# Performance work log

Measured on AMD Instinct MI355X. Metric: run time of the kernel, lower is better.

The kernel has to match this reference:

```python
import jax, jax.numpy as jnp
import numpy as np

B, N, D, K = 8, 262144, 16, 256
M_MAX = 1024  # cap on condensation points per event for the pairwise repulsion block
ATTR_W, REP_W = 1.0, 1.0
BETA_POS_W, BETA_NEG_SIG_W, BETA_NEG_BG_W, MARGIN_W = 10.0, 3.0, 6.0, 10.0
THR, MARGIN = 0.5, 0.3
ALPHA, GAMMA = 0.75, 2.0


def setup_inputs() -> dict:
    key = jax.random.key(0)
    k1, k2, k3, k4 = jax.random.split(key, 4)
    beta = jax.random.normal(k1, (B, N, 1), jnp.float32)
    embed = jax.random.normal(k2, (B, N, D), jnp.float32)
    slice_id = jax.random.randint(k3, (B, N), -1, K)          # -1 == background
    is_cp = jax.random.uniform(k4, (B, N)) < 0.001            # sparse condensation points
    return {"beta": beta, "embed": embed, "slice_id": slice_id, "is_cp": is_cp}


def _per_event(beta, emb, sid, cp):
    # beta [N], emb [N,D], sid [N] int, cp [N] bool
    f32 = beta.dtype
    valid = sid >= 0
    cpv = cp & valid
    seg = jnp.where(valid, sid, K).astype(jnp.int32)          # slot K = invalid/background bucket

    p = jax.nn.sigmoid(beta)
    ce1 = jax.nn.softplus(-beta)   # BCE-with-logits, target = 1
    ce0 = jax.nn.softplus(beta)    # BCE-with-logits, target = 0

    # ---- pos_bce: size-weighted per-instance focal BCE over CP hits ----
    focal = ALPHA * (1.0 - p) ** GAMMA * ce1
    cpf = cp.astype(f32)
    sum_f = jax.ops.segment_sum(focal * cpf, seg, num_segments=K + 1)[:K]
    cnt_cp = jax.ops.segment_sum(cpf, seg, num_segments=K + 1)[:K]
    inst_size = jax.ops.segment_sum(jnp.ones_like(beta), seg, num_segments=K + 1)[:K]
    has_cp = cnt_cp > 0
    mean_f = sum_f / jnp.maximum(cnt_cp, 1.0)
    w = jnp.where(has_cp, inst_size, 0.0)
    pos_bce = jnp.sum(w * mean_f) / jnp.maximum(jnp.sum(w), 1.0)

    # ---- negative / background BCE and margin terms ----
    ncpf = (~cp).astype(f32)
    n_ncp = jnp.sum(ncpf)
    neg_bce = jnp.where(n_ncp > 0, jnp.sum(ce0 * ncpf) / jnp.maximum(n_ncp, 1.0), 0.0)
    n_cp = jnp.sum(cpf)
    pos_margin = jnp.sum(jax.nn.relu(THR + MARGIN - p) * cpf) / jnp.maximum(n_cp, 1.0)
    neg_margin = jnp.where(n_ncp > 0,
                           jnp.sum(jax.nn.relu(p - (THR - MARGIN)) * ncpf) / jnp.maximum(n_ncp, 1.0), 0.0)
    bgf = (sid == -1).astype(f32)
    n_bg = jnp.sum(bgf)
    bg_bce = jnp.where(n_bg > 0, jnp.sum(ce0 * bgf) / jnp.maximum(n_bg, 1.0), 0.0)

    beta_loss = (BETA_POS_W * pos_bce + BETA_NEG_SIG_W * neg_bce +
                 BETA_NEG_BG_W * bg_bce + MARGIN_W * (pos_margin + neg_margin))

    # ---- attraction: per-instance mean sq-dist to the FIRST CP hit of that instance ----
    idx = jnp.where(cp, jnp.arange(N), N)
    first_idx = jax.ops.segment_min(idx, seg, num_segments=K + 1)[:K]   # N if instance has no CP
    anchor_k = emb[jnp.clip(first_idx, 0, N - 1)]                       # [K,D]
    anchor = anchor_k[jnp.clip(sid, 0, K - 1)]                          # [N,D]
    d2 = jnp.sum((emb - anchor) ** 2, axis=-1)
    s_d2 = jax.ops.segment_sum(d2 * valid.astype(f32), seg, num_segments=K + 1)[:K]
    attraction = ATTR_W * jnp.sum(jnp.where(has_cp, s_d2 / jnp.maximum(inst_size, 1.0), 0.0))

    # ---- repulsion: mean exp(-||ci-cj||^2) over all CP x CP pairs (incl. diagonal) ----
    order = jnp.argsort(jnp.where(cpv, jnp.arange(N), N))[:M_MAX]
    selv = cpv[order].astype(f32)                                       # [M]
    cp_emb = emb[order]                                                 # [M,D]
    pd2 = jnp.sum((cp_emb[:, None, :] - cp_emb[None, :, :]) ** 2, axis=-1)
    Mv = jnp.sum(cpv.astype(f32))
    rep = jnp.sum(jnp.exp(-pd2) * (selv[:, None] * selv[None, :])) / jnp.maximum(Mv * Mv, 1.0)
    repulsion = jnp.where(Mv > 1, REP_W * rep, 0.0)

    loss = beta_loss + attraction + repulsion
    ok = (jnp.sum(valid) > 0) & (Mv > 0)
    return loss, ok


def reference(beta, embed, slice_id, is_cp):
    beta2 = beta[..., 0]  # squeeze(-1)
    loss_b, ok_b = jax.vmap(_per_event)(beta2, embed, slice_id, is_cp)
    cnt = jnp.sum(ok_b.astype(beta2.dtype))
    total = jnp.sum(jnp.where(ok_b, loss_b, 0.0))
    return jnp.where(cnt > 0, total / jnp.maximum(cnt, 1.0), 0.0)
```

## Files before the change

### kernel.cpp

```cpp
#include <hip/hip_runtime.h>
#include <math.h>

#define Bn 8
#define Nn 262144
#define Kk 256
#define Dd 16
#define MCAP 4096
#define MSEL 1024
#define CHUNK 4096
#define ASTRIDE 17

#define W_ATTR 1.0f
#define W_REP 1.0f
#define W_BPOS 10.0f
#define W_BNEG 3.0f
#define W_BBG 6.0f
#define W_MARG 10.0f
#define ALPHA_F 0.75f

#define OFF_SUMF   0
#define OFF_CNT    (Bn*Kk)
#define OFF_INST   (2*Bn*Kk)
#define OFF_FIRST  (3*Bn*Kk)
#define OFF_SD2    (4*Bn*Kk)
#define OFF_ANCH   (5*Bn*Kk)
#define OFF_SCAL   (OFF_ANCH + Bn*Kk*Dd)
#define OFF_CPIDX  (OFF_SCAL + Bn*16)
#define OFF_MODE   (OFF_CPIDX + Bn*MCAP)
#define WS_WORDS   (OFF_MODE + 1)

__global__ void k_init(int* wsi) {
  int stride = gridDim.x * blockDim.x;
  for (int i = blockIdx.x * blockDim.x + threadIdx.x; i < WS_WORDS; i += stride) {
    int v = 0;
    if (i >= OFF_FIRST && i < OFF_FIRST + Bn * Kk) v = 0x7FFFFFFF;
    wsi[i] = v;
  }
}

__global__ void k_detect(const unsigned int* w, int* wsi) {
  int stride = gridDim.x * blockDim.x;
  int bad = 0;
  for (int i = blockIdx.x * blockDim.x + threadIdx.x; i < (Bn * Nn) / 4; i += stride) {
    unsigned int x = w[i];
    if (x > 1u && x != 0x3F800000u) bad = 1;
  }
  if (bad) atomicOr(&wsi[OFF_MODE], 1);
}

__global__ __launch_bounds__(256) void k_pass1(const float* __restrict__ beta,
                                               const int* __restrict__ sid,
                                               const void* __restrict__ cpp,
                                               float* wsf, int* wsi) {
  const int b = blockIdx.y;
  const int tid = threadIdx.x;
  __shared__ float ls_sumf[Kk];
  __shared__ int ls_cnt[Kk], ls_inst[Kk], ls_first[Kk];
  __shared__ float sr[4][4];
  __shared__ float si[4][2];
  ls_sumf[tid] = 0.f; ls_cnt[tid] = 0; ls_inst[tid] = 0; ls_first[tid] = 0x7FFFFFFF;
  __syncthreads();
  const int mode = wsi[OFF_MODE];
  const int base = b * Nn;
  const int i0 = blockIdx.x * CHUNK;
  float a_ce0n = 0.f, a_rpos = 0.f, a_rneg = 0.f, a_ce0b = 0.f;
  float a_ncp = 0.f, a_nbg = 0.f;
  for (int it = 0; it < CHUNK / 256; ++it) {
    int i = i0 + it * 256 + tid;
    int s = sid[base + i];
    bool cp;
    if (mode) cp = ((const unsigned char*)cpp)[base + i] != 0;
    else      cp = ((const unsigned int*)cpp)[base + i] != 0u;
    float x = beta[base + i];
    float p = 1.f / (1.f + __expf(-x));
    float ax = fabsf(x);
    float sp = log1pf(__expf(-ax));
    float ce1 = sp + fmaxf(-x, 0.f);
    float ce0 = sp + fmaxf(x, 0.f);
    if (cp) { a_rpos += fmaxf(0.8f - p, 0.f); a_ncp += 1.f; }
    else { a_ce0n += ce0; a_rneg += fmaxf(p - 0.2f, 0.f); }
    if (s == -1) { a_ce0b += ce0; a_nbg += 1.f; }
    if (s >= 0) {
      atomicAdd(&ls_inst[s], 1);
      if (cp) {
        float om = 1.f - p;
        float focal = ALPHA_F * om * om * ce1;
        atomicAdd(&ls_sumf[s], focal);
        atomicAdd(&ls_cnt[s], 1);
        atomicMin(&ls_first[s], i);
        int pos = atomicAdd(&wsi[OFF_SCAL + b * 16 + 6], 1);
        if (pos < MCAP) wsi[OFF_CPIDX + b * MCAP + pos] = i;
      }
    }
  }
  __syncthreads();
  atomicAdd(&wsf[OFF_SUMF + b * Kk + tid], ls_sumf[tid]);
  atomicAdd(&wsi[OFF_CNT + b * Kk + tid], ls_cnt[tid]);
  atomicAdd(&wsi[OFF_INST + b * Kk + tid], ls_inst[tid]);
  atomicMin(&wsi[OFF_FIRST + b * Kk + tid], ls_first[tid]);
  for (int o = 32; o > 0; o >>= 1) {
    a_ce0n += __shfl_down(a_ce0n, o);
    a_rpos += __shfl_down(a_rpos, o);
    a_rneg += __shfl_down(a_rneg, o);
    a_ce0b += __shfl_down(a_ce0b, o);
    a_ncp  += __shfl_down(a_ncp, o);
    a_nbg  += __shfl_down(a_nbg, o);
  }
  int wv = tid >> 6;
  if ((tid & 63) == 0) {
    sr[wv][0] = a_ce0n; sr[wv][1] = a_rpos; sr[wv][2] = a_rneg; sr[wv][3] = a_ce0b;
    si[wv][0] = a_ncp;  si[wv][1] = a_nbg;
  }
  __syncthreads();
  if (tid == 0) {
    float s0 = 0, s1 = 0, s2 = 0, s3 = 0, s4 = 0, s5 = 0;
    for (int wq = 0; wq < 4; ++wq) {
      s0 += sr[wq][0]; s1 += sr[wq][1]; s2 += sr[wq][2]; s3 += sr[wq][3];
      s4 += si[wq][0]; s5 += si[wq][1];
    }
    atomicAdd(&wsf[OFF_SCAL + b * 16 + 0], s0);
    atomicAdd(&wsf[OFF_SCAL + b * 16 + 1], s1);
    atomicAdd(&wsf[OFF_SCAL + b * 16 + 2], s2);
    atomicAdd(&wsf[OFF_SCAL + b * 16 + 3], s3);
    atomicAdd(&wsf[OFF_SCAL + b * 16 + 4], s4);
    atomicAdd(&wsf[OFF_SCAL + b * 16 + 5], s5);
  }
}

__global__ __launch_bounds__(256) void k_event(const float* __restrict__ embed,
                                               float* wsf, int* wsi) {
  const int b = blockIdx.x;
  const int t = threadIdx.x;
  int cnt = wsi[OFF_CNT + b * Kk + t];
  int inst = wsi[OFF_INST + b * Kk + t];
  float sf = wsf[OFF_SUMF + b * Kk + t];
  int fi = wsi[OFF_FIRST + b * Kk + t];
  bool has = cnt > 0;
  float w = has ? (float)inst : 0.f;
  float wf = has ? w * (sf / fmaxf((float)cnt, 1.f)) : 0.f;
  if (has) {
    const float4* src = (const float4*)(embed + ((size_t)b * Nn + (size_t)fi) * Dd);
    float4* dst = (float4*)(wsf + OFF_ANCH + ((size_t)b * Kk + t) * Dd);
    dst[0] = src[0]; dst[1] = src[1]; dst[2] = src[2]; dst[3] = src[3];
  }
  for (int o = 32; o > 0; o >>= 1) { w += __shfl_down(w, o); wf += __shfl_down(wf, o); }
  __shared__ float rw[4], rwf[4];
  if ((t & 63) == 0) { rw[t >> 6] = w; rwf[t >> 6] = wf; }
  __syncthreads();
  if (t == 0) {
    float sw = rw[0] + rw[1] + rw[2] + rw[3];
    float swf = rwf[0] + rwf[1] + rwf[2] + rwf[3];
    float pos_bce = swf / fmaxf(sw, 1.f);
    float ce0n = wsf[OFF_SCAL + b * 16 + 0];
    float rpos = wsf[OFF_SCAL + b * 16 + 1];
    float rneg = wsf[OFF_SCAL + b * 16 + 2];
    float ce0b = wsf[OFF_SCAL + b * 16 + 3];
    float ncp  = wsf[OFF_SCAL + b * 16 + 4];
    float nbg  = wsf[OFF_SCAL + b * 16 + 5];
    int mv = wsi[OFF_SCAL + b * 16 + 6];
    float nncp = (float)Nn - ncp;
    float neg_bce = nncp > 0.f ? ce0n / fmaxf(nncp, 1.f) : 0.f;
    float pos_m = rpos / fmaxf(ncp, 1.f);
    float neg_m = nncp > 0.f ? rneg / fmaxf(nncp, 1.f) : 0.f;
    float bg_bce = nbg > 0.f ? ce0b / fmaxf(nbg, 1.f) : 0.f;
    float bl = W_BPOS * pos_bce + W_BNEG * neg_bce + W_BBG * bg_bce + W_MARG * (pos_m + neg_m);
    wsf[OFF_SCAL + b * 16 + 8] = bl;
    float nvalid = (float)Nn - nbg;
    wsi[OFF_SCAL + b * 16 + 7] = (nvalid > 0.f && mv > 0) ? 1 : 0;
  }
}

__global__ __launch_bounds__(256) void k_rep(const float* __restrict__ embed,
                                             float* wsf, int* wsi) {
  const int b = blockIdx.x;
  const int t = threadIdx.x;
  __shared__ int sidx[MCAP];
  __shared__ float colT[256 * Dd];
  __shared__ float ra[4];
  const int mv = wsi[OFF_SCAL + b * 16 + 6];
  const int msel = mv < MSEL ? mv : MSEL;
  const int mload = mv < MCAP ? mv : MCAP;
  for (int i = t; i < MCAP; i += 256)
    sidx[i] = (i < mload) ? wsi[OFF_CPIDX + b * MCAP + i] : 0x7FFFFFFF;
  __syncthreads();
  if (mv > MSEL) {
    for (int ksz = 2; ksz <= MCAP; ksz <<= 1) {
      for (int j = ksz >> 1; j > 0; j >>= 1) {
        for (int e = t; e < MCAP; e += 256) {
          int ixj = e ^ j;
          if (ixj > e) {
            bool up = ((e & ksz) == 0);
            int a = sidx[e], c = sidx[ixj];
            if ((a > c) == up) { sidx[e] = c; sidx[ixj] = a; }
          }
        }
        __syncthreads();
      }
    }
  }
  const float* eb = embed + (size_t)b * Nn * Dd;
  float acc = 0.f;
  for (int r0 = 0; r0 < msel; r0 += 256) {
    int i = r0 + t;
    bool rok = i < msel;
    float e[Dd];
    if (rok) {
      const float4* s = (const float4*)(eb + (size_t)sidx[i] * Dd);
      float4 v0 = s[0], v1 = s[1], v2 = s[2], v3 = s[3];
      e[0]=v0.x; e[1]=v0.y; e[2]=v0.z; e[3]=v0.w;
      e[4]=v1.x; e[5]=v1.y; e[6]=v1.z; e[7]=v1.w;
      e[8]=v2.x; e[9]=v2.y; e[10]=v2.z; e[11]=v2.w;
      e[12]=v3.x; e[13]=v3.y; e[14]=v3.z; e[15]=v3.w;
    }
    for (int c0 = 0; c0 < msel; c0 += 256) {
      int nc = (msel - c0) < 256 ? (msel - c0) : 256;
      __syncthreads();
      for (int c = t; c < nc; c += 256) {
        const float4* s = (const float4*)(eb + (size_t)sidx[c0 + c] * Dd);
        float4* d = (float4*)&colT[c * Dd];
        d[0] = s[0]; d[1] = s[1]; d[2] = s[2]; d[3] = s[3];
      }
      __syncthreads();
      if (rok) {
        for (int c = 0; c < nc; ++c) {
          float d2 = 0.f;
          #pragma unroll
          for (int d = 0; d < Dd; ++d) {
            float df = e[d] - colT[c * Dd + d];
            d2 += df * df;
          }
          acc += __expf(-d2);
        }
      }
    }
  }
  for (int o = 32; o > 0; o >>= 1) acc += __shfl_down(acc, o);
  if ((t & 63) == 0) ra[t >> 6] = acc;
  __syncthreads();
  if (t == 0) {
    float s = ra[0] + ra[1] + ra[2] + ra[3];
    float mvf = (float)mv;
    wsf[OFF_SCAL + b * 16 + 9] = (mv > 1) ? (W_REP * s / fmaxf(mvf * mvf, 1.f)) : 0.f;
  }
}

__global__ __launch_bounds__(256) void k_attr(const float* __restrict__ embed,
                                              const int* __restrict__ sid,
                                              float* wsf, int* wsi) {
  const int b = blockIdx.y;
  const int tid = threadIdx.x;
  __shared__ float anch[Kk * ASTRIDE];
  __shared__ int hasf[Kk];
  __shared__ float ld2[Kk];
  const float* ga = wsf + OFF_ANCH + (size_t)b * Kk * Dd;
  for (int i = tid; i < Kk * Dd; i += 256) {
    int k = i >> 4, d = i & 15;
    anch[k * ASTRIDE + d] = ga[i];
  }
  hasf[tid] = (wsi[OFF_CNT + b * Kk + tid] > 0) ? 1 : 0;
  ld2[tid] = 0.f;
  __syncthreads();
  const int base = b * Nn;
  const float* eb = embed + (size_t)base * Dd;
  const int i0 = blockIdx.x * CHUNK;
  for (int it = 0; it < CHUNK / 256; ++it) {
    int i = i0 + it * 256 + tid;
    int s = sid[base + i];
    if (s >= 0 && hasf[s]) {
      const float4* e4 = (const float4*)(eb + (size_t)i * Dd);
      float4 v0 = e4[0], v1 = e4[1], v2 = e4[2], v3 = e4[3];
      const float* a = &anch[s * ASTRIDE];
      float d2 = 0.f, df;
      df = v0.x - a[0];  d2 += df * df;
      df = v0.y - a[1];  d2 += df * df;
      df = v0.z - a[2];  d2 += df * df;
      df = v0.w - a[3];  d2 += df * df;
      df = v1.x - a[4];  d2 += df * df;
      df = v1.y - a[5];  d2 += df * df;
      df = v1.z - a[6];  d2 += df * df;
      df = v1.w - a[7];  d2 += df * df;
      df = v2.x - a[8];  d2 += df * df;
      df = v2.y - a[9];  d2 += df * df;
      df = v2.z - a[10]; d2 += df * df;
      df = v2.w - a[11]; d2 += df * df;
      df = v3.x - a[12]; d2 += df * df;
      df = v3.y - a[13]; d2 += df * df;
      df = v3.z - a[14]; d2 += df * df;
      df = v3.w - a[15]; d2 += df * df;
      atomicAdd(&ld2[s], d2);
    }
  }
  __syncthreads();
  atomicAdd(&wsf[OFF_SD2 + b * Kk + tid], ld2[tid]);
}

__global__ __launch_bounds__(256) void k_final(float* wsf, int* wsi, float* out, int out_size) {
  __shared__ float att[Bn];
  const int t = threadIdx.x;
  if (t < Bn) att[t] = 0.f;
  __syncthreads();
  for (int i = t; i < Bn * Kk; i += 256) {
    int bb = i >> 8;
    if (wsi[OFF_CNT + i] > 0) {
      float inst = (float)wsi[OFF_INST + i];
      float v = wsf[OFF_SD2 + i] / fmaxf(inst, 1.f);
      atomicAdd(&att[bb], v);
    }
  }
  __syncthreads();
  if (t == 0) {
    float total = 0.f;
    int cnt = 0;
    for (int bb = 0; bb < Bn; ++bb) {
      if (wsi[OFF_SCAL + bb * 16 + 7]) {
        total += wsf[OFF_SCAL + bb * 16 + 8] + W_ATTR * att[bb] + wsf[OFF_SCAL + bb * 16 + 9];
        cnt++;
      }
    }
    out[0] = (cnt > 0) ? total / (float)cnt : 0.f;
  }
  for (int i = t + 1; i < out_size; i += 256) out[i] = 0.f;
}

extern "C" void kernel_launch(void* const* d_in, const int* in_sizes, int n_in,
                              void* d_out, int out_size, void* d_ws, size_t ws_size,
                              hipStream_t stream) {
  const float* beta = (const float*)d_in[0];
  const float* embed = (const float*)d_in[1];
  const int* sid = (const int*)d_in[2];
  const void* cp = d_in[3];
  float* out = (float*)d_out;
  float* wsf = (float*)d_ws;
  int* wsi = (int*)d_ws;

  k_init<<<128, 256, 0, stream>>>(wsi);
  k_detect<<<256, 256, 0, stream>>>((const unsigned int*)cp, wsi);
  dim3 g1(Nn / CHUNK, Bn);
  k_pass1<<<g1, 256, 0, stream>>>(beta, sid, cp, wsf, wsi);
  k_event<<<Bn, 256, 0, stream>>>(embed, wsf, wsi);
  k_rep<<<Bn, 256, 0, stream>>>(embed, wsf, wsi);
  k_attr<<<g1, 256, 0, stream>>>(embed, sid, wsf, wsi);
  k_final<<<1, 256, 0, stream>>>(wsf, wsi, out, out_size);
}
```

Before: 328.3 us.

## Fuse attraction into main pass via sum/sumsq expansion and parallelize repulsion

```diff
diff --git a/kernel.cpp b/kernel.cpp
--- a/kernel.cpp
+++ b/kernel.cpp
@@ -8,7 +8,8 @@
 #define MCAP 4096
 #define MSEL 1024
 #define CHUNK 4096
-#define ASTRIDE 17
+#define ESTR 17
+#define CSTR 20
 
 #define W_ATTR 1.0f
 #define W_REP 1.0f
@@ -18,25 +19,16 @@
 #define W_MARG 10.0f
 #define ALPHA_F 0.75f
 
-#define OFF_SUMF   0
-#define OFF_CNT    (Bn*Kk)
-#define OFF_INST   (2*Bn*Kk)
-#define OFF_FIRST  (3*Bn*Kk)
-#define OFF_SD2    (4*Bn*Kk)
-#define OFF_ANCH   (5*Bn*Kk)
-#define OFF_SCAL   (OFF_ANCH + Bn*Kk*Dd)
-#define OFF_CPIDX  (OFF_SCAL + Bn*16)
-#define OFF_MODE   (OFF_CPIDX + Bn*MCAP)
-#define WS_WORDS   (OFF_MODE + 1)
-
-__global__ void k_init(int* wsi) {
-  int stride = gridDim.x * blockDim.x;
-  for (int i = blockIdx.x * blockDim.x + threadIdx.x; i < WS_WORDS; i += stride) {
-    int v = 0;
-    if (i >= OFF_FIRST && i < OFF_FIRST + Bn * Kk) v = 0x7FFFFFFF;
-    wsi[i] = v;
-  }
-}
+#define OFF_SUMF 0
+#define OFF_CNT 2048
+#define OFF_INST 4096
+#define OFF_ESQ 6144
+#define OFF_SCAL 8192
+#define OFF_MODE 8448
+#define OFF_ESUM 8464
+#define ZERO_WORDS (8464 + Bn*Kk*Dd)
+#define OFF_FIRST ZERO_WORDS
+#define OFF_CPIDX (OFF_FIRST + Bn*Kk)
 
 __global__ void k_detect(const unsigned int* w, int* wsi) {
   int stride = gridDim.x * blockDim.x;
@@ -48,82 +40,114 @@
   if (bad) atomicOr(&wsi[OFF_MODE], 1);
 }
 
-__global__ __launch_bounds__(256) void k_pass1(const float* __restrict__ beta,
-                                               const int* __restrict__ sid,
-                                               const void* __restrict__ cpp,
-                                               float* wsf, int* wsi) {
+__global__ __launch_bounds__(256) void k_pass(const float* __restrict__ beta,
+                                              const int* __restrict__ sid,
+                                              const void* __restrict__ cpp,
+                                              const float* __restrict__ embed,
+                                              float* wsf, int* wsi) {
   const int b = blockIdx.y;
   const int tid = threadIdx.x;
-  __shared__ float ls_sumf[Kk];
-  __shared__ int ls_cnt[Kk], ls_inst[Kk], ls_first[Kk];
-  __shared__ float sr[4][4];
-  __shared__ float si[4][2];
-  ls_sumf[tid] = 0.f; ls_cnt[tid] = 0; ls_inst[tid] = 0; ls_first[tid] = 0x7FFFFFFF;
+  __shared__ float ls_esum[Kk * ESTR];
+  __shared__ float ls_esq[Kk], ls_sumf[Kk];
+  __shared__ int ls_inst[Kk], ls_cnt[Kk], ls_first[Kk];
+  __shared__ float sred[4][8];
+  for (int i = tid; i < Kk * ESTR; i += 256) ls_esum[i] = 0.f;
+  ls_esq[tid] = 0.f; ls_sumf[tid] = 0.f;
+  ls_inst[tid] = 0; ls_cnt[tid] = 0; ls_first[tid] = 0x7FFFFFFF;
   __syncthreads();
   const int mode = wsi[OFF_MODE];
   const int base = b * Nn;
-  const int i0 = blockIdx.x * CHUNK;
-  float a_ce0n = 0.f, a_rpos = 0.f, a_rneg = 0.f, a_ce0b = 0.f;
-  float a_ncp = 0.f, a_nbg = 0.f;
-  for (int it = 0; it < CHUNK / 256; ++it) {
-    int i = i0 + it * 256 + tid;
-    int s = sid[base + i];
-    bool cp;
-    if (mode) cp = ((const unsigned char*)cpp)[base + i] != 0;
-    else      cp = ((const unsigned int*)cpp)[base + i] != 0u;
-    float x = beta[base + i];
-    float p = 1.f / (1.f + __expf(-x));
-    float ax = fabsf(x);
-    float sp = log1pf(__expf(-ax));
-    float ce1 = sp + fmaxf(-x, 0.f);
-    float ce0 = sp + fmaxf(x, 0.f);
-    if (cp) { a_rpos += fmaxf(0.8f - p, 0.f); a_ncp += 1.f; }
-    else { a_ce0n += ce0; a_rneg += fmaxf(p - 0.2f, 0.f); }
-    if (s == -1) { a_ce0b += ce0; a_nbg += 1.f; }
-    if (s >= 0) {
-      atomicAdd(&ls_inst[s], 1);
-      if (cp) {
-        float om = 1.f - p;
-        float focal = ALPHA_F * om * om * ce1;
-        atomicAdd(&ls_sumf[s], focal);
-        atomicAdd(&ls_cnt[s], 1);
-        atomicMin(&ls_first[s], i);
-        int pos = atomicAdd(&wsi[OFF_SCAL + b * 16 + 6], 1);
-        if (pos < MCAP) wsi[OFF_CPIDX + b * MCAP + pos] = i;
+  const float* eb = embed + (size_t)base * Dd;
+  float a0 = 0.f, a1 = 0.f, a2 = 0.f, a3 = 0.f, a4 = 0.f, a5 = 0.f;
+  for (int it = 0; it < CHUNK / 1024; ++it) {
+    const int i0 = blockIdx.x * CHUNK + it * 1024 + tid * 4;
+    int4 s4 = *(const int4*)(sid + base + i0);
+    float4 b4 = *(const float4*)(beta + base + i0);
+    unsigned int cpw[4];
+    if (mode) {
+      unsigned int u = ((const unsigned int*)cpp)[(base + i0) >> 2];
+      cpw[0] = u & 0xffu; cpw[1] = (u >> 8) & 0xffu;
+      cpw[2] = (u >> 16) & 0xffu; cpw[3] = u >> 24;
+    } else {
+      uint4 u = ((const uint4*)cpp)[(base + i0) >> 2];
+      cpw[0] = u.x; cpw[1] = u.y; cpw[2] = u.z; cpw[3] = u.w;
+    }
+    const int ss[4] = {s4.x, s4.y, s4.z, s4.w};
+    const float xs[4] = {b4.x, b4.y, b4.z, b4.w};
+    #pragma unroll
+    for (int j = 0; j < 4; ++j) {
+      const int s = ss[j];
+      const bool cp = cpw[j] != 0u;
+      const float x = xs[j];
+      const float p = 1.f / (1.f + __expf(-x));
+      const float ax = fabsf(x);
+      const float sp = __logf(1.f + __expf(-ax));
+      const float ce0 = sp + fmaxf(x, 0.f);
+      if (cp) { a1 += fmaxf(0.8f - p, 0.f); a4 += 1.f; }
+      else    { a0 += ce0; a2 += fmaxf(p - 0.2f, 0.f); }
+      if (s == -1) { a3 += ce0; a5 += 1.f; }
+      if (s >= 0) {
+        atomicAdd(&ls_inst[s], 1);
+        const int i = i0 + j;
+        const float4* e4 = (const float4*)(eb + (size_t)i * Dd);
+        float4 v0 = e4[0], v1 = e4[1], v2 = e4[2], v3 = e4[3];
+        float esq = v0.x*v0.x + v0.y*v0.y + v0.z*v0.z + v0.w*v0.w
+                  + v1.x*v1.x + v1.y*v1.y + v1.z*v1.z + v1.w*v1.w
+                  + v2.x*v2.x + v2.y*v2.y + v2.z*v2.z + v2.w*v2.w
+                  + v3.x*v3.x + v3.y*v3.y + v3.z*v3.z + v3.w*v3.w;
+        atomicAdd(&ls_esq[s], esq);
+        float* es = &ls_esum[s * ESTR];
+        atomicAdd(&es[0],  v0.x); atomicAdd(&es[1],  v0.y);
+        atomicAdd(&es[2],  v0.z); atomicAdd(&es[3],  v0.w);
+        atomicAdd(&es[4],  v1.x); atomicAdd(&es[5],  v1.y);
+        atomicAdd(&es[6],  v1.z); atomicAdd(&es[7],  v1.w);
+        atomicAdd(&es[8],  v2.x); atomicAdd(&es[9],  v2.y);
+        atomicAdd(&es[10], v2.z); atomicAdd(&es[11], v2.w);
+        atomicAdd(&es[12], v3.x); atomicAdd(&es[13], v3.y);
+        atomicAdd(&es[14], v3.z); atomicAdd(&es[15], v3.w);
+        if (cp) {
+          const float ce1 = sp + fmaxf(-x, 0.f);
+          const float om = 1.f - p;
+          atomicAdd(&ls_sumf[s], ALPHA_F * om * om * ce1);
+          atomicAdd(&ls_cnt[s], 1);
+          atomicMin(&ls_first[s], i);
+          int pos = atomicAdd(&wsi[OFF_SCAL + b * 32 + 6], 1);
+          if (pos < MCAP) wsi[OFF_CPIDX + b * MCAP + pos] = i;
+        }
       }
     }
   }
   __syncthreads();
   atomicAdd(&wsf[OFF_SUMF + b * Kk + tid], ls_sumf[tid]);
-  atomicAdd(&wsi[OFF_CNT + b * Kk + tid], ls_cnt[tid]);
+  if (ls_cnt[tid]) atomicAdd(&wsi[OFF_CNT + b * Kk + tid], ls_cnt[tid]);
   atomicAdd(&wsi[OFF_INST + b * Kk + tid], ls_inst[tid]);
+  atomicAdd(&wsf[OFF_ESQ + b * Kk + tid], ls_esq[tid]);
   atomicMin(&wsi[OFF_FIRST + b * Kk + tid], ls_first[tid]);
+  #pragma unroll
+  for (int d = 0; d < Dd; ++d)
+    atomicAdd(&wsf[OFF_ESUM + ((size_t)b * Kk + tid) * Dd + d], ls_esum[tid * ESTR + d]);
   for (int o = 32; o > 0; o >>= 1) {
-    a_ce0n += __shfl_down(a_ce0n, o);
-    a_rpos += __shfl_down(a_rpos, o);
-    a_rneg += __shfl_down(a_rneg, o);
-    a_ce0b += __shfl_down(a_ce0b, o);
-    a_ncp  += __shfl_down(a_ncp, o);
-    a_nbg  += __shfl_down(a_nbg, o);
-  }
-  int wv = tid >> 6;
+    a0 += __shfl_down(a0, o); a1 += __shfl_down(a1, o); a2 += __shfl_down(a2, o);
+    a3 += __shfl_down(a3, o); a4 += __shfl_down(a4, o); a5 += __shfl_down(a5, o);
+  }
+  const int wv = tid >> 6;
   if ((tid & 63) == 0) {
-    sr[wv][0] = a_ce0n; sr[wv][1] = a_rpos; sr[wv][2] = a_rneg; sr[wv][3] = a_ce0b;
-    si[wv][0] = a_ncp;  si[wv][1] = a_nbg;
+    sred[wv][0] = a0; sred[wv][1] = a1; sred[wv][2] = a2;
+    sred[wv][3] = a3; sred[wv][4] = a4; sred[wv][5] = a5;
   }
   __syncthreads();
   if (tid == 0) {
     float s0 = 0, s1 = 0, s2 = 0, s3 = 0, s4 = 0, s5 = 0;
-    for (int wq = 0; wq < 4; ++wq) {
-      s0 += sr[wq][0]; s1 += sr[wq][1]; s2 += sr[wq][2]; s3 += sr[wq][3];
-      s4 += si[wq][0]; s5 += si[wq][1];
-    }
-    atomicAdd(&wsf[OFF_SCAL + b * 16 + 0], s0);
-    atomicAdd(&wsf[OFF_SCAL + b * 16 + 1], s1);
-    atomicAdd(&wsf[OFF_SCAL + b * 16 + 2], s2);
-    atomicAdd(&wsf[OFF_SCAL + b * 16 + 3], s3);
-    atomicAdd(&wsf[OFF_SCAL + b * 16 + 4], s4);
-    atomicAdd(&wsf[OFF_SCAL + b * 16 + 5], s5);
+    for (int q = 0; q < 4; ++q) {
+      s0 += sred[q][0]; s1 += sred[q][1]; s2 += sred[q][2];
+      s3 += sred[q][3]; s4 += sred[q][4]; s5 += sred[q][5];
+    }
+    atomicAdd(&wsf[OFF_SCAL + b * 32 + 0], s0);
+    atomicAdd(&wsf[OFF_SCAL + b * 32 + 1], s1);
+    atomicAdd(&wsf[OFF_SCAL + b * 32 + 2], s2);
+    atomicAdd(&wsf[OFF_SCAL + b * 32 + 3], s3);
+    atomicAdd(&wsf[OFF_SCAL + b * 32 + 4], s4);
+    atomicAdd(&wsf[OFF_SCAL + b * 32 + 5], s5);
   }
 }
 
@@ -131,53 +155,69 @@
                                                float* wsf, int* wsi) {
   const int b = blockIdx.x;
   const int t = threadIdx.x;
-  int cnt = wsi[OFF_CNT + b * Kk + t];
-  int inst = wsi[OFF_INST + b * Kk + t];
-  float sf = wsf[OFF_SUMF + b * Kk + t];
-  int fi = wsi[OFF_FIRST + b * Kk + t];
-  bool has = cnt > 0;
-  float w = has ? (float)inst : 0.f;
-  float wf = has ? w * (sf / fmaxf((float)cnt, 1.f)) : 0.f;
+  const int cnt = wsi[OFF_CNT + b * Kk + t];
+  const int inst = wsi[OFF_INST + b * Kk + t];
+  const float sumf = wsf[OFF_SUMF + b * Kk + t];
+  const int fi = wsi[OFF_FIRST + b * Kk + t];
+  const float esq = wsf[OFF_ESQ + b * Kk + t];
+  const float4* ep = (const float4*)(wsf + OFF_ESUM + ((size_t)b * Kk + t) * Dd);
+  float4 S0 = ep[0], S1 = ep[1], S2 = ep[2], S3 = ep[3];
+  const bool has = cnt > 0;
+  float attr_p = 0.f, w = 0.f, wf = 0.f;
   if (has) {
-    const float4* src = (const float4*)(embed + ((size_t)b * Nn + (size_t)fi) * Dd);
-    float4* dst = (float4*)(wsf + OFF_ANCH + ((size_t)b * Kk + t) * Dd);
-    dst[0] = src[0]; dst[1] = src[1]; dst[2] = src[2]; dst[3] = src[3];
-  }
-  for (int o = 32; o > 0; o >>= 1) { w += __shfl_down(w, o); wf += __shfl_down(wf, o); }
-  __shared__ float rw[4], rwf[4];
-  if ((t & 63) == 0) { rw[t >> 6] = w; rwf[t >> 6] = wf; }
+    const float4* a4 = (const float4*)(embed + ((size_t)b * Nn + (size_t)fi) * Dd);
+    float4 A0 = a4[0], A1 = a4[1], A2 = a4[2], A3 = a4[3];
+    float asq = A0.x*A0.x + A0.y*A0.y + A0.z*A0.z + A0.w*A0.w
+              + A1.x*A1.x + A1.y*A1.y + A1.z*A1.z + A1.w*A1.w
+              + A2.x*A2.x + A2.y*A2.y + A2.z*A2.z + A2.w*A2.w
+              + A3.x*A3.x + A3.y*A3.y + A3.z*A3.z + A3.w*A3.w;
+    float ad = A0.x*S0.x + A0.y*S0.y + A0.z*S0.z + A0.w*S0.w
+             + A1.x*S1.x + A1.y*S1.y + A1.z*S1.z + A1.w*S1.w
+             + A2.x*S2.x + A2.y*S2.y + A2.z*S2.z + A2.w*S2.w
+             + A3.x*S3.x + A3.y*S3.y + A3.z*S3.z + A3.w*S3.w;
+    const float instf = (float)inst;
+    const float d2s = esq - 2.f * ad + instf * asq;
+    attr_p = d2s / fmaxf(instf, 1.f);
+    w = instf;
+    wf = instf * (sumf / fmaxf((float)cnt, 1.f));
+  }
+  for (int o = 32; o > 0; o >>= 1) {
+    attr_p += __shfl_down(attr_p, o);
+    w += __shfl_down(w, o);
+    wf += __shfl_down(wf, o);
+  }
+  __shared__ float r3[3][4];
+  if ((t & 63) == 0) { r3[0][t >> 6] = attr_p; r3[1][t >> 6] = w; r3[2][t >> 6] = wf; }
   __syncthreads();
   if (t == 0) {
-    float sw = rw[0] + rw[1] + rw[2] + rw[3];
-    float swf = rwf[0] + rwf[1] + rwf[2] + rwf[3];
+    float at = r3[0][0] + r3[0][1] + r3[0][2] + r3[0][3];
+    float sw = r3[1][0] + r3[1][1] + r3[1][2] + r3[1][3];
+    float swf = r3[2][0] + r3[2][1] + r3[2][2] + r3[2][3];
     float pos_bce = swf / fmaxf(sw, 1.f);
-    float ce0n = wsf[OFF_SCAL + b * 16 + 0];
-    float rpos = wsf[OFF_SCAL + b * 16 + 1];
-    float rneg = wsf[OFF_SCAL + b * 16 + 2];
-    float ce0b = wsf[OFF_SCAL + b * 16 + 3];
-    float ncp  = wsf[OFF_SCAL + b * 16 + 4];
-    float nbg  = wsf[OFF_SCAL + b * 16 + 5];
-    int mv = wsi[OFF_SCAL + b * 16 + 6];
+    float* sc = wsf + OFF_SCAL + b * 32;
+    float ce0n = sc[0], rpos = sc[1], rneg = sc[2], ce0b = sc[3], ncp = sc[4], nbg = sc[5];
+    int mv = wsi[OFF_SCAL + b * 32 + 6];
     float nncp = (float)Nn - ncp;
     float neg_bce = nncp > 0.f ? ce0n / fmaxf(nncp, 1.f) : 0.f;
     float pos_m = rpos / fmaxf(ncp, 1.f);
     float neg_m = nncp > 0.f ? rneg / fmaxf(nncp, 1.f) : 0.f;
     float bg_bce = nbg > 0.f ? ce0b / fmaxf(nbg, 1.f) : 0.f;
-    float bl = W_BPOS * pos_bce + W_BNEG * neg_bce + W_BBG * bg_bce + W_MARG * (pos_m + neg_m);
-    wsf[OFF_SCAL + b * 16 + 8] = bl;
+    sc[8] = W_BPOS * pos_bce + W_BNEG * neg_bce + W_BBG * bg_bce + W_MARG * (pos_m + neg_m);
+    sc[10] = at;
     float nvalid = (float)Nn - nbg;
-    wsi[OFF_SCAL + b * 16 + 7] = (nvalid > 0.f && mv > 0) ? 1 : 0;
+    wsi[OFF_SCAL + b * 32 + 7] = (nvalid > 0.f && mv > 0) ? 1 : 0;
   }
 }
 
 __global__ __launch_bounds__(256) void k_rep(const float* __restrict__ embed,
                                              float* wsf, int* wsi) {
-  const int b = blockIdx.x;
+  const int b = blockIdx.y;
   const int t = threadIdx.x;
   __shared__ int sidx[MCAP];
-  __shared__ float colT[256 * Dd];
-  __shared__ float ra[4];
-  const int mv = wsi[OFF_SCAL + b * 16 + 6];
+  __shared__ float cemb[256 * CSTR];
+  __shared__ float csq[256];
+  __shared__ float red[4];
+  const int mv = wsi[OFF_SCAL + b * 32 + 6];
   const int msel = mv < MSEL ? mv : MSEL;
   const int mload = mv < MCAP ? mv : MCAP;
   for (int i = t; i < MCAP; i += 256)
@@ -190,8 +230,8 @@
           int ixj = e ^ j;
           if (ixj > e) {
             bool up = ((e & ksz) == 0);
-            int a = sidx[e], c = sidx[ixj];
-            if ((a > c) == up) { sidx[e] = c; sidx[ixj] = a; }
+            int x = sidx[e], y = sidx[ixj];
+            if ((x > y) == up) { sidx[e] = y; sidx[ixj] = x; }
           }
         }
         __syncthreads();
@@ -199,127 +239,75 @@
     }
   }
   const float* eb = embed + (size_t)b * Nn * Dd;
+  const int row = blockIdx.x * 64 + (t & 63);
+  const int cg = t >> 6;
+  const bool rok = row < msel;
+  float r[Dd];
+  float rsq = 0.f;
+  if (rok) {
+    const float4* s = (const float4*)(eb + (size_t)sidx[row] * Dd);
+    float4 v0 = s[0], v1 = s[1], v2 = s[2], v3 = s[3];
+    r[0]=v0.x; r[1]=v0.y; r[2]=v0.z; r[3]=v0.w;
+    r[4]=v1.x; r[5]=v1.y; r[6]=v1.z; r[7]=v1.w;
+    r[8]=v2.x; r[9]=v2.y; r[10]=v2.z; r[11]=v2.w;
+    r[12]=v3.x; r[13]=v3.y; r[14]=v3.z; r[15]=v3.w;
+    #pragma unroll
+    for (int d = 0; d < Dd; ++d) rsq += r[d] * r[d];
+  }
   float acc = 0.f;
-  for (int r0 = 0; r0 < msel; r0 += 256) {
-    int i = r0 + t;
-    bool rok = i < msel;
-    float e[Dd];
+  for (int c0 = 0; c0 < msel; c0 += 256) {
+    const int nc = (msel - c0) < 256 ? (msel - c0) : 256;
+    __syncthreads();
+    for (int wvi = t; wvi < nc * 4; wvi += 256) {
+      int col = wvi >> 2, q = wvi & 3;
+      float4 v = ((const float4*)(eb + (size_t)sidx[c0 + col] * Dd))[q];
+      *(float4*)&cemb[col * CSTR + q * 4] = v;
+    }
+    __syncthreads();
+    for (int col = t; col < nc; col += 256) {
+      float s = 0.f;
+      #pragma unroll
+      for (int d = 0; d < Dd; ++d) s += cemb[col * CSTR + d] * cemb[col * CSTR + d];
+      csq[col] = s;
+    }
+    __syncthreads();
     if (rok) {
-      const float4* s = (const float4*)(eb + (size_t)sidx[i] * Dd);
-      float4 v0 = s[0], v1 = s[1], v2 = s[2], v3 = s[3];
-      e[0]=v0.x; e[1]=v0.y; e[2]=v0.z; e[3]=v0.w;
-      e[4]=v1.x; e[5]=v1.y; e[6]=v1.z; e[7]=v1.w;
-      e[8]=v2.x; e[9]=v2.y; e[10]=v2.z; e[11]=v2.w;
-      e[12]=v3.x; e[13]=v3.y; e[14]=v3.z; e[15]=v3.w;
-    }
-    for (int c0 = 0; c0 < msel; c0 += 256) {
-      int nc = (msel - c0) < 256 ? (msel - c0) : 256;
-      __syncthreads();
-      for (int c = t; c < nc; c += 256) {
-        const float4* s = (const float4*)(eb + (size_t)sidx[c0 + c] * Dd);
-        float4* d = (float4*)&colT[c * Dd];
-        d[0] = s[0]; d[1] = s[1]; d[2] = s[2]; d[3] = s[3];
+      for (int c = cg; c < nc; c += 4) {
+        float dotrc = 0.f;
+        #pragma unroll
+        for (int d = 0; d < Dd; ++d) dotrc += r[d] * cemb[c * CSTR + d];
+        acc += __expf(2.f * dotrc - rsq - csq[c]);
       }
-      __syncthreads();
-      if (rok) {
-        for (int c = 0; c < nc; ++c) {
-          float d2 = 0.f;
-          #pragma unroll
-          for (int d = 0; d < Dd; ++d) {
-            float df = e[d] - colT[c * Dd + d];
-            d2 += df * df;
-          }
-          acc += __expf(-d2);
-        }
-      }
     }
   }
   for (int o = 32; o > 0; o >>= 1) acc += __shfl_down(acc, o);
-  if ((t & 63) == 0) ra[t >> 6] = acc;
+  if ((t & 63) == 0) red[t >> 6] = acc;
   __syncthreads();
   if (t == 0) {
-    float s = ra[0] + ra[1] + ra[2] + ra[3];
-    float mvf = (float)mv;
-    wsf[OFF_SCAL + b * 16 + 9] = (mv > 1) ? (W_REP * s / fmaxf(mvf * mvf, 1.f)) : 0.f;
-  }
-}
-
-__global__ __launch_bounds__(256) void k_attr(const float* __restrict__ embed,
-                                              const int* __restrict__ sid,
-                                              float* wsf, int* wsi) {
-  const int b = blockIdx.y;
-  const int tid = threadIdx.x;
-  __shared__ float anch[Kk * ASTRIDE];
-  __shared__ int hasf[Kk];
-  __shared__ float ld2[Kk];
-  const float* ga = wsf + OFF_ANCH + (size_t)b * Kk * Dd;
-  for (int i = tid; i < Kk * Dd; i += 256) {
-    int k = i >> 4, d = i & 15;
-    anch[k * ASTRIDE + d] = ga[i];
-  }
-  hasf[tid] = (wsi[OFF_CNT + b * Kk + tid] > 0) ? 1 : 0;
-  ld2[tid] = 0.f;
-  __syncthreads();
-  const int base = b * Nn;
-  const float* eb = embed + (size_t)base * Dd;
-  const int i0 = blockIdx.x * CHUNK;
-  for (int it = 0; it < CHUNK / 256; ++it) {
-    int i = i0 + it * 256 + tid;
-    int s = sid[base + i];
-    if (s >= 0 && hasf[s]) {
-      const float4* e4 = (const float4*)(eb + (size_t)i * Dd);
-      float4 v0 = e4[0], v1 = e4[1], v2 = e4[2], v3 = e4[3];
-      const float* a = &anch[s * ASTRIDE];
-      float d2 = 0.f, df;
-      df = v0.x - a[0];  d2 += df * df;
-      df = v0.y - a[1];  d2 += df * df;
-      df = v0.z - a[2];  d2 += df * df;
-      df = v0.w - a[3];  d2 += df * df;
-      df = v1.x - a[4];  d2 += df * df;
-      df = v1.y - a[5];  d2 += df * df;
-      df = v1.z - a[6];  d2 += df * df;
-      df = v1.w - a[7];  d2 += df * df;
-      df = v2.x - a[8];  d2 += df * df;
-      df = v2.y - a[9];  d2 += df * df;
-      df = v2.z - a[10]; d2 += df * df;
-      df = v2.w - a[11]; d2 += df * df;
-      df = v3.x - a[12]; d2 += df * df;
-      df = v3.y - a[13]; d2 += df * df;
-      df = v3.z - a[14]; d2 += df * df;
-      df = v3.w - a[15]; d2 += df * df;
-      atomicAdd(&ld2[s], d2);
-    }
-  }
-  __syncthreads();
-  atomicAdd(&wsf[OFF_SD2 + b * Kk + tid], ld2[tid]);
-}
-
-__global__ __launch_bounds__(256) void k_final(float* wsf, int* wsi, float* out, int out_size) {
-  __shared__ float att[Bn];
+    float s = red[0] + red[1] + red[2] + red[3];
+    if (s != 0.f) atomicAdd(&wsf[OFF_SCAL + b * 32 + 9], s);
+  }
+}
+
+__global__ void k_final(float* wsf, int* wsi, float* out, int out_size) {
   const int t = threadIdx.x;
-  if (t < Bn) att[t] = 0.f;
-  __syncthreads();
-  for (int i = t; i < Bn * Kk; i += 256) {
-    int bb = i >> 8;
-    if (wsi[OFF_CNT + i] > 0) {
-      float inst = (float)wsi[OFF_INST + i];
-      float v = wsf[OFF_SD2 + i] / fmaxf(inst, 1.f);
-      atomicAdd(&att[bb], v);
-    }
-  }
-  __syncthreads();
   if (t == 0) {
     float total = 0.f;
     int cnt = 0;
-    for (int bb = 0; bb < Bn; ++bb) {
-      if (wsi[OFF_SCAL + bb * 16 + 7]) {
-        total += wsf[OFF_SCAL + bb * 16 + 8] + W_ATTR * att[bb] + wsf[OFF_SCAL + bb * 16 + 9];
+    for (int b = 0; b < Bn; ++b) {
+      float* sc = wsf + OFF_SCAL + b * 32;
+      int* sci = wsi + OFF_SCAL + b * 32;
+      int mv = sci[6];
+      if (sci[7]) {
+        float mvf = (float)mv;
+        float rep = (mv > 1) ? W_REP * sc[9] / fmaxf(mvf * mvf, 1.f) : 0.f;
+        total += sc[8] + W_ATTR * sc[10] + rep;
         cnt++;
       }
     }
     out[0] = (cnt > 0) ? total / (float)cnt : 0.f;
   }
-  for (int i = t + 1; i < out_size; i += 256) out[i] = 0.f;
+  for (int i = 1 + t; i < out_size; i += 256) out[i] = 0.f;
 }
 
 extern "C" void kernel_launch(void* const* d_in, const int* in_sizes, int n_in,
@@ -333,12 +321,13 @@
   float* wsf = (float*)d_ws;
   int* wsi = (int*)d_ws;
 
-  k_init<<<128, 256, 0, stream>>>(wsi);
+  hipMemsetAsync(d_ws, 0, (size_t)ZERO_WORDS * 4, stream);
+  hipMemsetAsync((char*)d_ws + (size_t)OFF_FIRST * 4, 0x7F, (size_t)Bn * Kk * 4, stream);
   k_detect<<<256, 256, 0, stream>>>((const unsigned int*)cp, wsi);
-  dim3 g1(Nn / CHUNK, Bn);
-  k_pass1<<<g1, 256, 0, stream>>>(beta, sid, cp, wsf, wsi);
+  dim3 gp(Nn / CHUNK, Bn);
+  k_pass<<<gp, 256, 0, stream>>>(beta, sid, cp, embed, wsf, wsi);
   k_event<<<Bn, 256, 0, stream>>>(embed, wsf, wsi);
-  k_rep<<<Bn, 256, 0, stream>>>(embed, wsf, wsi);
-  k_attr<<<g1, 256, 0, stream>>>(embed, sid, wsf, wsi);
+  dim3 gr(MSEL / 64, Bn);
+  k_rep<<<gr, 256, 0, stream>>>(embed, wsf, wsi);
   k_final<<<1, 256, 0, stream>>>(wsf, wsi, out, out_size);
 }
```

Result: slower. 459.3 us (+39.9%).
